# Optimization experiments

Measured on AMD Instinct MI355X. Metric: run time of the kernel, lower is better.

Reference implementation:

```python
import jax, jax.numpy as jnp
import numpy as np


def setup_inputs() -> dict:
    key = jax.random.key(0)
    ks = jax.random.split(key, 7)
    B, T, D, H = 32, 512, 512, 512
    return {
        "x": jax.random.normal(ks[0], (B, T, D), dtype=jnp.float32),
        "W_Du": jax.random.normal(ks[1], (D, H), dtype=jnp.float32) * (1.0 / np.sqrt(D)),
        "W_Dr1": jax.random.normal(ks[2], (D, H), dtype=jnp.float32) * (1.0 / np.sqrt(D)),
        "W_Dr2": jax.random.normal(ks[3], (D, H), dtype=jnp.float32) * (1.0 / np.sqrt(D)),
        "b_Du": jax.random.normal(ks[4], (H,), dtype=jnp.float32) * 0.02,
        "b_Dr1": jax.random.normal(ks[5], (H,), dtype=jnp.float32) * 0.02,
        "b_Dr2": jax.random.normal(ks[6], (H,), dtype=jnp.float32) * 0.02,
    }


def reference(x, W_Du, W_Dr1, W_Dr2, b_Du, b_Dr1, b_Dr2):
    # Precompute all per-step projections across time (batched matmuls),
    # then run the strictly sequential gated recurrence with lax.scan.
    r1 = jax.nn.softmax(jnp.einsum('btd,dh->bth', x, W_Dr1) + b_Dr1, axis=-1)  # [B,T,H]
    r2 = jax.nn.softmax(jnp.einsum('btd,dh->bth', x, W_Dr2) + b_Dr2, axis=-1)  # [B,T,H]
    u = jnp.tanh(jnp.einsum('btd,dh->bth', x, W_Du) + b_Du)                     # [B,T,H]

    def step(s, inp):
        r1t, r2t, ut = inp
        s_new = r1t * s + r2t * ut
        return s_new, s_new

    init = jnp.zeros((x.shape[0], W_Du.shape[1]), dtype=x.dtype)
    # time-major for scan: [T,B,H]
    _, ys = jax.lax.scan(
        step, init,
        (jnp.swapaxes(r1, 0, 1), jnp.swapaxes(r2, 0, 1), jnp.swapaxes(u, 0, 1)),
    )
    return jnp.swapaxes(ys, 0, 1)  # [B,T,H]
```

## Files before the change

### kernel.cpp

```cpp
#include <hip/hip_runtime.h>
#include <hip/hip_bf16.h>

#define B_N 32
#define T_N 512
#define D_N 512
#define H_N 512
#define M_N (B_N * T_N)

typedef __attribute__((ext_vector_type(8))) short bf16x8;
typedef __attribute__((ext_vector_type(4))) float f32x4;

__device__ __forceinline__ unsigned short f2bf(float f) {
  unsigned u = __float_as_uint(f);
  u += 0x7FFFu + ((u >> 16) & 1u);
  return (unsigned short)(u >> 16);
}
__device__ __forceinline__ unsigned short f2h(float f) {
  _Float16 h = (_Float16)f;
  return *(unsigned short*)&h;
}
__device__ __forceinline__ float h2f(unsigned short u) {
  _Float16 h = *(_Float16*)&u;
  return (float)h;
}

#define GLOAD16(g, l) __builtin_amdgcn_global_load_lds( \
    (const __attribute__((address_space(1))) void*)(g), \
    (__attribute__((address_space(3))) void*)(l), 16, 0, 0)

__global__ void prep_kernel(const float* __restrict__ x,
                            const float* __restrict__ W0,
                            const float* __restrict__ W1,
                            const float* __restrict__ W2,
                            unsigned short* __restrict__ xb,
                            unsigned short* __restrict__ Wt,
                            float* __restrict__ S) {
  int blk = blockIdx.x;
  int tid = threadIdx.x;
  if (blk < 768) {
    __shared__ float tile[32][33];
    int id = blk >> 8;
    int t = blk & 255;
    int kr = (t >> 4) << 5;
    int nc = (t & 15) << 5;
    const float* W = (id == 0) ? W0 : (id == 1) ? W1 : W2;
    unsigned short* Wo = Wt + (size_t)id * (D_N * H_N);
    int tx = tid & 31, ty0 = tid >> 5;
    for (int ty = ty0; ty < 32; ty += 8)
      tile[ty][tx] = W[(size_t)(kr + ty) * H_N + nc + tx];
    __syncthreads();
    for (int ty = ty0; ty < 32; ty += 8)
      Wo[(size_t)(nc + ty) * D_N + kr + tx] = f2bf(tile[tx][ty]);
  } else if (blk < 2816) {
    int b = blk - 768;
    const float4* xv = (const float4*)x;
#pragma unroll
    for (int u = 0; u < 4; ++u) {
      int i = b * 1024 + u * 256 + tid;
      float4 v = xv[i];
      ushort4 o;
      o.x = f2bf(v.x); o.y = f2bf(v.y); o.z = f2bf(v.z); o.w = f2bf(v.w);
      ((ushort4*)xb)[i] = o;
    }
  } else {
    ((float4*)S)[(blk - 2816) * 256 + tid] = (float4){0.f, 0.f, 0.f, 0.f};
  }
}

__global__ __launch_bounds__(256, 4) void gemm3(
    const unsigned short* __restrict__ xb,
    const unsigned short* __restrict__ Wt,
    const float* __restrict__ bDu,
    const float* __restrict__ bDr1,
    const float* __restrict__ bDr2,
    unsigned short* __restrict__ uP,
    unsigned short* __restrict__ e1P,
    unsigned short* __restrict__ e2P,
    float* __restrict__ S1,
    float* __restrict__ S2) {
  __shared__ __align__(16) char smem[32768];

  const int wg = (blockIdx.x & 7) * 192 + (blockIdx.x >> 3);
  const int bx = wg / 12;
  const int rzy = wg - bx * 12;
  const int id = rzy >> 2;
  const int by = rzy & 3;

  const int tid = threadIdx.x;
  const int lane = tid & 63;
  const int wv = tid >> 6;
  const int wr = wv >> 1;
  const int wc = wv & 1;
  const int g = lane >> 4;
  const int c16 = lane & 15;

  const int m0 = bx * 128;
  const int n0 = by * 128;
  const unsigned short* Wp = Wt + (size_t)id * (D_N * H_N);

  f32x4 acc[4][4];
#pragma unroll
  for (int mt = 0; mt < 4; ++mt)
#pragma unroll
    for (int nt = 0; nt < 4; ++nt)
      acc[mt][nt] = (f32x4){0.f, 0.f, 0.f, 0.f};

  const int rowoff = tid >> 3;
  const int lsl = ((tid & 7) ^ ((tid >> 3) & 7)) * 8;
  const unsigned short* aSrc = xb + (size_t)(m0 + rowoff) * D_N + lsl;
  const unsigned short* bSrc = Wp + (size_t)(n0 + rowoff) * D_N + lsl;
  const int dstOff = wv * 1024;

  const int h3 = c16 & 7;

#pragma unroll 1
  for (int t = 0; t < 8; ++t) {
    const int k0 = t * 64;
#pragma unroll
    for (int i = 0; i < 4; ++i)
      GLOAD16(aSrc + (size_t)i * (32 * D_N) + k0, smem + dstOff + i * 4096);
#pragma unroll
    for (int i = 0; i < 4; ++i)
      GLOAD16(bSrc + (size_t)i * (32 * D_N) + k0,
              smem + 16384 + dstOff + i * 4096);
    __syncthreads();
#pragma unroll
    for (int kh = 0; kh < 2; ++kh) {
      const int soff = ((kh * 4 + g) ^ h3) << 4;
      bf16x8 bb[4];
#pragma unroll
      for (int nt = 0; nt < 4; ++nt)
        bb[nt] = *(const bf16x8*)(smem + 16384 +
                                  (wc * 64 + nt * 16 + c16) * 128 + soff);
#pragma unroll
      for (int mt = 0; mt < 4; ++mt) {
        bf16x8 af = *(const bf16x8*)(smem +
                                     (wr * 64 + mt * 16 + c16) * 128 + soff);
#pragma unroll
        for (int nt = 0; nt < 4; ++nt)
          acc[mt][nt] = __builtin_amdgcn_mfma_f32_16x16x32_bf16(
              af, bb[nt], acc[mt][nt], 0, 0, 0);
      }
    }
    __syncthreads();
  }

  const float* bp = (id == 0) ? bDu : (id == 1) ? bDr1 : bDr2;
  unsigned short* outp = (id == 0) ? uP : (id == 1) ? e1P : e2P;
  float* Sp = (id == 1) ? S1 : S2;
  float bias[4];
#pragma unroll
  for (int nt = 0; nt < 4; ++nt)
    bias[nt] = bp[n0 + wc * 64 + nt * 16 + c16];

#pragma unroll
  for (int mt = 0; mt < 4; ++mt)
#pragma unroll
    for (int i = 0; i < 4; ++i) {
      int row = m0 + wr * 64 + mt * 16 + g * 4 + i;
      unsigned short* op = outp + (size_t)row * H_N + n0 + wc * 64 + c16;
      if (id == 0) {
#pragma unroll
        for (int nt = 0; nt < 4; ++nt) {
          float z = acc[mt][nt][i] + bias[nt];
          float e = __expf(2.f * z);
          op[nt * 16] = f2h(1.f - 2.f * __builtin_amdgcn_rcpf(e + 1.f));
        }
      } else {
        float ps = 0.f;
#pragma unroll
        for (int nt = 0; nt < 4; ++nt) {
          float e = __expf(acc[mt][nt][i] + bias[nt]);
          op[nt * 16] = f2h(e);
          ps += e;
        }
        ps += __shfl_xor(ps, 1);
        ps += __shfl_xor(ps, 2);
        ps += __shfl_xor(ps, 4);
        ps += __shfl_xor(ps, 8);
        if (c16 == 0) atomicAdd(&Sp[row], ps);
      }
    }
}

__global__ void scan_pass1(const unsigned short* __restrict__ e1P,
                           const unsigned short* __restrict__ e2P,
                           const unsigned short* __restrict__ uP,
                           const float* __restrict__ S1,
                           const float* __restrict__ S2,
                           float* __restrict__ cP,
                           float* __restrict__ cS) {
  __shared__ float ls1[64], ls2[64];
  int gt = blockIdx.x * 256 + threadIdx.x;
  int chunk = gt >> 14;
  int r = gt & 16383;
  int b = r >> 9, h = r & 511;
  int row0 = b * T_N + chunk * 64;
  if (threadIdx.x < 64) ls1[threadIdx.x] = 1.f / S1[row0 + threadIdx.x];
  else if (threadIdx.x < 128) ls2[threadIdx.x - 64] = 1.f / S2[row0 + threadIdx.x - 64];
  __syncthreads();
  size_t idx = (size_t)row0 * H_N + h;
  float p = 1.f, s = 0.f;
#pragma unroll 4
  for (int j = 0; j < 64; ++j) {
    float a = ls1[j] * h2f(e1P[idx]);
    float cu = ls2[j] * h2f(e2P[idx]) * h2f(uP[idx]);
    s = fmaf(a, s, cu);
    p *= a;
    idx += H_N;
  }
  cP[gt] = p;
  cS[gt] = s;
}

__global__ void scan_pass3(const unsigned short* __restrict__ e1P,
                           const unsigned short* __restrict__ e2P,
                           const unsigned short* __restrict__ uP,
                           const float* __restrict__ S1,
                           const float* __restrict__ S2,
                           const float* __restrict__ cP,
                           const float* __restrict__ cS,
                           float* __restrict__ out) {
  __shared__ float ls1[64], ls2[64];
  int gt = blockIdx.x * 256 + threadIdx.x;
  int chunk = gt >> 14;
  int r = gt & 16383;
  int b = r >> 9, h = r & 511;
  int row0 = b * T_N + chunk * 64;
  if (threadIdx.x < 64) ls1[threadIdx.x] = 1.f / S1[row0 + threadIdx.x];
  else if (threadIdx.x < 128) ls2[threadIdx.x - 64] = 1.f / S2[row0 + threadIdx.x - 64];
  float s = 0.f;
  for (int c2 = 0; c2 < chunk; ++c2)
    s = fmaf(cP[c2 * 16384 + r], s, cS[c2 * 16384 + r]);
  __syncthreads();
  size_t idx = (size_t)row0 * H_N + h;
#pragma unroll 4
  for (int j = 0; j < 64; ++j) {
    float a = ls1[j] * h2f(e1P[idx]);
    float cu = ls2[j] * h2f(e2P[idx]) * h2f(uP[idx]);
    s = fmaf(a, s, cu);
    out[idx] = s;
    idx += H_N;
  }
}

extern "C" void kernel_launch(void* const* d_in, const int* in_sizes, int n_in,
                              void* d_out, int out_size, void* d_ws, size_t ws_size,
                              hipStream_t stream) {
  const float* x  = (const float*)d_in[0];
  const float* W0 = (const float*)d_in[1];
  const float* W1 = (const float*)d_in[2];
  const float* W2 = (const float*)d_in[3];
  const float* b0 = (const float*)d_in[4];
  const float* b1 = (const float*)d_in[5];
  const float* b2 = (const float*)d_in[6];
  float* out = (float*)d_out;

  char* ws = (char*)d_ws;
  unsigned short* xb  = (unsigned short*)ws;
  unsigned short* Wt  = (unsigned short*)(ws + 16777216);
  unsigned short* uP  = (unsigned short*)(ws + 18350080);
  unsigned short* e1P = (unsigned short*)(ws + 35127296);
  unsigned short* e2P = (unsigned short*)(ws + 51904512);
  float*          S1  = (float*)(ws + 68681728);
  float*          S2  = (float*)(ws + 68747264);
  float*          cP  = (float*)(ws + 68812800);
  float*          cS  = (float*)(ws + 69337088);

  prep_kernel<<<2848, 256, 0, stream>>>(x, W0, W1, W2, xb, Wt, S1);
  gemm3<<<1536, 256, 0, stream>>>(xb, Wt, b0, b1, b2, uP, e1P, e2P, S1, S2);
  scan_pass1<<<512, 256, 0, stream>>>(e1P, e2P, uP, S1, S2, cP, cS);
  scan_pass3<<<512, 256, 0, stream>>>(e1P, e2P, uP, S1, S2, cP, cS, out);
}
```

Before: 81.64 us.

## Load GEMM A fragments directly from global and vectorize scan kernels over two columns

The GEMM no longer stages the x tile through LDS. Each wave loads its A fragments straight from global memory into registers, which halves shared memory and drops the launch-bounds occupancy hint. The two scan kernels now have each thread handle two adjacent hidden columns with paired half and float loads and stores, which halves the thread and block count. The tradeoffs are uncoalesced A reads that are duplicated across waves, higher register pressure in the GEMM, and fewer blocks in the scan, which leaves less parallelism to hide latency.

After: 104.2 us. 1.28x slower.

```diff
diff --git a/kernel.cpp b/kernel.cpp
--- a/kernel.cpp
+++ b/kernel.cpp
@@ -67,7 +67,7 @@
   }
 }
 
-__global__ __launch_bounds__(256, 4) void gemm3(
+__global__ void gemm3(
     const unsigned short* __restrict__ xb,
     const unsigned short* __restrict__ Wt,
     const float* __restrict__ bDu,
@@ -78,7 +78,7 @@
     unsigned short* __restrict__ e2P,
     float* __restrict__ S1,
     float* __restrict__ S2) {
-  __shared__ __align__(16) char smem[32768];
+  __shared__ __align__(16) char smem[16384];
 
   const int wg = (blockIdx.x & 7) * 192 + (blockIdx.x >> 3);
   const int bx = wg / 12;
@@ -107,9 +107,11 @@
 
   const int rowoff = tid >> 3;
   const int lsl = ((tid & 7) ^ ((tid >> 3) & 7)) * 8;
-  const unsigned short* aSrc = xb + (size_t)(m0 + rowoff) * D_N + lsl;
   const unsigned short* bSrc = Wp + (size_t)(n0 + rowoff) * D_N + lsl;
   const int dstOff = wv * 1024;
+
+  const unsigned short* aBase =
+      xb + (size_t)(m0 + wr * 64 + c16) * D_N + g * 8;
 
   const int h3 = c16 & 7;
 
@@ -118,11 +120,14 @@
     const int k0 = t * 64;
 #pragma unroll
     for (int i = 0; i < 4; ++i)
-      GLOAD16(aSrc + (size_t)i * (32 * D_N) + k0, smem + dstOff + i * 4096);
-#pragma unroll
-    for (int i = 0; i < 4; ++i)
-      GLOAD16(bSrc + (size_t)i * (32 * D_N) + k0,
-              smem + 16384 + dstOff + i * 4096);
+      GLOAD16(bSrc + (size_t)i * (32 * D_N) + k0, smem + dstOff + i * 4096);
+    bf16x8 af[2][4];
+#pragma unroll
+    for (int kh = 0; kh < 2; ++kh)
+#pragma unroll
+      for (int mt = 0; mt < 4; ++mt)
+        af[kh][mt] = *(const bf16x8*)(aBase + (size_t)(mt * 16) * D_N +
+                                      k0 + kh * 32);
     __syncthreads();
 #pragma unroll
     for (int kh = 0; kh < 2; ++kh) {
@@ -130,17 +135,14 @@
       bf16x8 bb[4];
 #pragma unroll
       for (int nt = 0; nt < 4; ++nt)
-        bb[nt] = *(const bf16x8*)(smem + 16384 +
+        bb[nt] = *(const bf16x8*)(smem +
                                   (wc * 64 + nt * 16 + c16) * 128 + soff);
 #pragma unroll
-      for (int mt = 0; mt < 4; ++mt) {
-        bf16x8 af = *(const bf16x8*)(smem +
-                                     (wr * 64 + mt * 16 + c16) * 128 + soff);
+      for (int mt = 0; mt < 4; ++mt)
 #pragma unroll
         for (int nt = 0; nt < 4; ++nt)
           acc[mt][nt] = __builtin_amdgcn_mfma_f32_16x16x32_bf16(
-              af, bb[nt], acc[mt][nt], 0, 0, 0);
-      }
+              af[kh][mt], bb[nt], acc[mt][nt], 0, 0, 0);
     }
     __syncthreads();
   }
@@ -192,25 +194,32 @@
                            float* __restrict__ cS) {
   __shared__ float ls1[64], ls2[64];
   int gt = blockIdx.x * 256 + threadIdx.x;
-  int chunk = gt >> 14;
-  int r = gt & 16383;
-  int b = r >> 9, h = r & 511;
+  int chunk = gt >> 13;
+  int r = gt & 8191;
+  int b = r >> 8, hp = r & 255;
+  int h = hp * 2;
   int row0 = b * T_N + chunk * 64;
   if (threadIdx.x < 64) ls1[threadIdx.x] = 1.f / S1[row0 + threadIdx.x];
   else if (threadIdx.x < 128) ls2[threadIdx.x - 64] = 1.f / S2[row0 + threadIdx.x - 64];
   __syncthreads();
   size_t idx = (size_t)row0 * H_N + h;
-  float p = 1.f, s = 0.f;
+  float p0 = 1.f, s0 = 0.f, p1 = 1.f, s1 = 0.f;
 #pragma unroll 4
   for (int j = 0; j < 64; ++j) {
-    float a = ls1[j] * h2f(e1P[idx]);
-    float cu = ls2[j] * h2f(e2P[idx]) * h2f(uP[idx]);
-    s = fmaf(a, s, cu);
-    p *= a;
+    ushort2 v1 = *(const ushort2*)(e1P + idx);
+    ushort2 v2 = *(const ushort2*)(e2P + idx);
+    ushort2 vu = *(const ushort2*)(uP + idx);
+    float i1 = ls1[j], i2 = ls2[j];
+    float a0 = i1 * h2f(v1.x), a1 = i1 * h2f(v1.y);
+    s0 = fmaf(a0, s0, i2 * h2f(v2.x) * h2f(vu.x));
+    s1 = fmaf(a1, s1, i2 * h2f(v2.y) * h2f(vu.y));
+    p0 *= a0;
+    p1 *= a1;
     idx += H_N;
   }
-  cP[gt] = p;
-  cS[gt] = s;
+  int base = chunk * 16384 + b * 512 + h;
+  *(float2*)(cP + base) = (float2){p0, p1};
+  *(float2*)(cS + base) = (float2){s0, s1};
 }
 
 __global__ void scan_pass3(const unsigned short* __restrict__ e1P,
@@ -223,23 +232,33 @@
                            float* __restrict__ out) {
   __shared__ float ls1[64], ls2[64];
   int gt = blockIdx.x * 256 + threadIdx.x;
-  int chunk = gt >> 14;
-  int r = gt & 16383;
-  int b = r >> 9, h = r & 511;
+  int chunk = gt >> 13;
+  int r = gt & 8191;
+  int b = r >> 8, hp = r & 255;
+  int h = hp * 2;
   int row0 = b * T_N + chunk * 64;
   if (threadIdx.x < 64) ls1[threadIdx.x] = 1.f / S1[row0 + threadIdx.x];
   else if (threadIdx.x < 128) ls2[threadIdx.x - 64] = 1.f / S2[row0 + threadIdx.x - 64];
-  float s = 0.f;
-  for (int c2 = 0; c2 < chunk; ++c2)
-    s = fmaf(cP[c2 * 16384 + r], s, cS[c2 * 16384 + r]);
+  int rr = b * 512 + h;
+  float s0 = 0.f, s1 = 0.f;
+  for (int c2 = 0; c2 < chunk; ++c2) {
+    float2 pp = *(const float2*)(cP + c2 * 16384 + rr);
+    float2 ss = *(const float2*)(cS + c2 * 16384 + rr);
+    s0 = fmaf(pp.x, s0, ss.x);
+    s1 = fmaf(pp.y, s1, ss.y);
+  }
   __syncthreads();
   size_t idx = (size_t)row0 * H_N + h;
 #pragma unroll 4
   for (int j = 0; j < 64; ++j) {
-    float a = ls1[j] * h2f(e1P[idx]);
-    float cu = ls2[j] * h2f(e2P[idx]) * h2f(uP[idx]);
-    s = fmaf(a, s, cu);
-    out[idx] = s;
+    ushort2 v1 = *(const ushort2*)(e1P + idx);
+    ushort2 v2 = *(const ushort2*)(e2P + idx);
+    ushort2 vu = *(const ushort2*)(uP + idx);
+    float i1 = ls1[j], i2 = ls2[j];
+    float a0 = i1 * h2f(v1.x), a1 = i1 * h2f(v1.y);
+    s0 = fmaf(a0, s0, i2 * h2f(v2.x) * h2f(vu.x));
+    s1 = fmaf(a1, s1, i2 * h2f(v2.y) * h2f(vu.y));
+    *(float2*)(out + idx) = (float2){s0, s1};
     idx += H_N;
   }
 }
@@ -269,6 +288,6 @@
 
   prep_kernel<<<2848, 256, 0, stream>>>(x, W0, W1, W2, xb, Wt, S1);
   gemm3<<<1536, 256, 0, stream>>>(xb, Wt, b0, b1, b2, uP, e1P, e2P, S1, S2);
-  scan_pass1<<<512, 256, 0, stream>>>(e1P, e2P, uP, S1, S2, cP, cS);
-  scan_pass3<<<512, 256, 0, stream>>>(e1P, e2P, uP, S1, S2, cP, cS, out);
-}
+  scan_pass1<<<256, 256, 0, stream>>>(e1P, e2P, uP, S1, S2, cP, cS);
+  scan_pass3<<<256, 256, 0, stream>>>(e1P, e2P, uP, S1, S2, cP, cS, out);
+}
```
